# Kernel optimization log

Measured on AMD Instinct MI355X. Metric: run time of the kernel, lower is better.

The kernel has to match this reference:

```python
import jax, jax.numpy as jnp
import numpy as np

NEG_INF = -1e30

def _rotate_half(x):
    x1, x2 = jnp.split(x, 2, axis=-1)
    return jnp.concatenate([-x2, x1], axis=-1)

def _apply_rope(x, sin, cos):
    # x: [b, t, h, d]; sin/cos: [t, d]
    s = sin[None, :, None, :]
    c = cos[None, :, None, :]
    return x * c + _rotate_half(x) * s

def setup_inputs() -> dict:
    key = jax.random.key(0)
    ks = jax.random.split(key, 5)
    B, T, D, H = 2, 2048, 2048, 16
    hd = D // H
    x = jax.random.normal(ks[0], (B, T, D), dtype=jnp.float32)
    sin = jax.random.normal(ks[1], (T, hd), dtype=jnp.float32)
    cos = jax.random.normal(ks[2], (T, hd), dtype=jnp.float32)
    W_qkv = jax.random.normal(ks[3], (D, D + 2 * hd), dtype=jnp.float32) * (1.0 / np.sqrt(D))
    W_o = jax.random.normal(ks[4], (D, D), dtype=jnp.float32) * (1.0 / np.sqrt(D))
    return {"x": x, "sin": sin, "cos": cos, "W_qkv": W_qkv, "W_o": W_o}

def reference(x, sin, cos, W_qkv, W_o):
    B, T, D = x.shape
    num_heads = 16
    head_dim = D // num_heads
    scale = head_dim ** (-0.5)

    qkv = x @ W_qkv                              # [B, T, D + 2*hd]
    q, k, v = jnp.split(qkv, [D, D + head_dim], axis=-1)
    # q -> [B, H, T, hd]; k, v single KV head -> [B, 1, T, hd]
    q = q.reshape(B, T, num_heads, head_dim).transpose(0, 2, 1, 3)
    k = k[:, :, None, :].transpose(0, 2, 1, 3)   # [B, 1, T, hd]
    v = v[:, :, None, :].transpose(0, 2, 1, 3)

    # module scales q by head_dim^-0.5 BEFORE rope/attention
    q = q * scale

    # apply_rope_safe: transpose to [B, T, H, hd], apply rope, transpose back
    q = _apply_rope(q.transpose(0, 2, 1, 3), sin, cos).transpose(0, 2, 1, 3)
    k = _apply_rope(k.transpose(0, 2, 1, 3), sin, cos).transpose(0, 2, 1, 3)

    k0 = k[:, 0]                                 # [B, T, hd] (MQA shared KV)
    v0 = v[:, 0]

    # jax.nn.dot_product_attention applies its own 1/sqrt(hd) scaling on top
    scores = jnp.einsum('bhqd,bkd->bhqk', q, k0) * scale
    causal = jnp.tril(jnp.ones((T, T), dtype=bool))
    scores = jnp.where(causal[None, None], scores, NEG_INF)
    probs = jax.nn.softmax(scores, axis=-1)
    out = jnp.einsum('bhqk,bkd->bhqd', probs, v0)  # [B, H, T, hd]

    out = out.transpose(0, 2, 1, 3).reshape(B, T, D)
    return out @ W_o
```

## Files before the change

kernel.cpp:

```cpp
#include <hip/hip_runtime.h>
#include <stdint.h>

typedef __bf16 bf16x8_t __attribute__((ext_vector_type(8)));
typedef float f32x4_t __attribute__((ext_vector_type(4)));

#define AS1 __attribute__((address_space(1)))
#define AS3 __attribute__((address_space(3)))

static __device__ __forceinline__ unsigned short f2bf(float f) {
  union { float f; unsigned u; } a;
  a.f = f;
  unsigned r = a.u + 0x7fffu + ((a.u >> 16) & 1u);
  return (unsigned short)(r >> 16);
}

static __device__ __forceinline__ unsigned pack2bf(float lo, float hi) {
  return (unsigned)f2bf(lo) | ((unsigned)f2bf(hi) << 16);
}

__global__ void cvt_bf16_kernel(const float* __restrict__ in, unsigned short* __restrict__ out) {
  long i = ((long)blockIdx.x * blockDim.x + threadIdx.x) * 4;
  float4 v = *(const float4*)(in + i);
  ushort4 o;
  o.x = f2bf(v.x);
  o.y = f2bf(v.y);
  o.z = f2bf(v.z);
  o.w = f2bf(v.w);
  *(ushort4*)(out + i) = o;
}

__global__ void transpose_f32_bf16(const float* __restrict__ src, unsigned short* __restrict__ dst,
                                   int ld, int dld, long sbs, long dbs) {
  __shared__ float tile[64][65];
  src += (long)blockIdx.z * sbs;
  dst += (long)blockIdx.z * dbs;
  const int c0 = blockIdx.x * 64, r0 = blockIdx.y * 64;
  const int tx = threadIdx.x, ty = threadIdx.y;
#pragma unroll
  for (int j = 0; j < 64; j += 4)
    tile[ty + j][tx] = src[(long)(r0 + ty + j) * ld + (c0 + tx)];
  __syncthreads();
#pragma unroll
  for (int j = 0; j < 64; j += 4)
    dst[(long)(c0 + ty + j) * dld + (r0 + tx)] = f2bf(tile[tx][ty + j]);
}

__global__ __launch_bounds__(256) void gemm_bt(const unsigned short* __restrict__ A,
                                               const unsigned short* __restrict__ Bt,
                                               float* __restrict__ C,
                                               int M, int N, int K, int nx) {
  __shared__ unsigned short As[3][128 * 32];
  __shared__ unsigned short Bs[3][128 * 32];
  const int nwg = gridDim.x;
  const int bid = blockIdx.x;
  const int swz = (bid & 7) * (nwg >> 3) + (bid >> 3);
  const int by = swz / nx;
  const int bx = swz - by * nx;

  const int tid = threadIdx.x;
  const int wid = tid >> 6, lane = tid & 63;
  const int r16 = lane & 15, g = lane >> 4;
  const long bm = (long)by * 128;
  const long bn = (long)bx * 128;
  const int wr = (wid >> 1) * 64, wc = (wid & 1) * 64;
  const int gr = g ^ (r16 & 3);
  const int sslot = (lane & 3) ^ ((lane >> 2) & 3);

  f32x4_t acc[4][4];
#pragma unroll
  for (int i = 0; i < 4; i++)
#pragma unroll
    for (int j = 0; j < 4; j++) acc[i][j] = (f32x4_t){0.f, 0.f, 0.f, 0.f};

  const int NT = K >> 5;

#define STAGE_G(buf, kt)                                                              \
  {                                                                                   \
    _Pragma("unroll") for (int i = 0; i < 2; i++) {                                   \
      const int chunk = (i * 4 + wid) * 64 + lane;                                    \
      const int row = chunk >> 2;                                                     \
      __builtin_amdgcn_global_load_lds(                                               \
          (const AS1 void*)(A + (bm + row) * K + (kt) + sslot * 8),                   \
          (AS3 void*)(&As[buf][chunk * 8]), 16, 0, 0);                                \
      __builtin_amdgcn_global_load_lds(                                               \
          (const AS1 void*)(Bt + (bn + row) * K + (kt) + sslot * 8),                  \
          (AS3 void*)(&Bs[buf][chunk * 8]), 16, 0, 0);                                \
    }                                                                                 \
  }

  STAGE_G(0, 0)
  STAGE_G(1, 32)
  asm volatile("s_waitcnt vmcnt(4)" ::: "memory");
  __builtin_amdgcn_s_barrier();

  for (int T = 0; T < NT; T++) {
    const int cur = T % 3;
    if (T + 2 < NT) {
      const int nb = (T + 2) % 3;
      STAGE_G(nb, (T + 2) * 32)
    }
    __builtin_amdgcn_sched_barrier(0);
    bf16x8_t af[4], bfr[4];
#pragma unroll
    for (int mi = 0; mi < 4; mi++)
      af[mi] = *(const bf16x8_t*)(&As[cur][(wr + mi * 16 + r16) * 32 + gr * 8]);
#pragma unroll
    for (int ni = 0; ni < 4; ni++)
      bfr[ni] = *(const bf16x8_t*)(&Bs[cur][(wc + ni * 16 + r16) * 32 + gr * 8]);
    __builtin_amdgcn_s_setprio(1);
#pragma unroll
    for (int mi = 0; mi < 4; mi++)
#pragma unroll
      for (int ni = 0; ni < 4; ni++)
        acc[mi][ni] = __builtin_amdgcn_mfma_f32_16x16x32_bf16(af[mi], bfr[ni], acc[mi][ni], 0, 0, 0);
    __builtin_amdgcn_s_setprio(0);
    if (T + 2 < NT)
      asm volatile("s_waitcnt vmcnt(4)" ::: "memory");
    else
      asm volatile("s_waitcnt vmcnt(0)" ::: "memory");
    __builtin_amdgcn_s_barrier();
  }
#undef STAGE_G

#pragma unroll
  for (int mi = 0; mi < 4; mi++)
#pragma unroll
    for (int ni = 0; ni < 4; ni++) {
      const long rowb = bm + wr + mi * 16 + 4 * g;
      const long colb = bn + wc + ni * 16 + r16;
#pragma unroll
      for (int j = 0; j < 4; j++)
        C[(rowb + j) * N + colb] = acc[mi][ni][j];
    }
}

__global__ void rope_kernel(const float* __restrict__ qkv,
                            const float* __restrict__ sinp,
                            const float* __restrict__ cosp,
                            unsigned short* __restrict__ qr,
                            unsigned short* __restrict__ kr) {
  const int row = blockIdx.x;
  const int b = row >> 11, t = row & 2047;
  const float* src = qkv + (long)row * 2304;
  const int tid = threadIdx.x;
  const int d = tid & 127;
  const int dp = (d + 64) & 127;
  const float c = cosp[t * 128 + d];
  const float s = sinp[t * 128 + d];
  const float sgn = (d < 64) ? -1.f : 1.f;
  for (int h = (tid >> 7); h < 16; h += 2) {
    const float x0 = src[h * 128 + d];
    const float xp = src[h * 128 + dp];
    qr[((long)((b * 16 + h) * 2048 + t)) * 128 + d] = f2bf((x0 * c + sgn * xp * s) * 0.0078125f);
  }
  if (tid < 128) {
    const float x0 = src[2048 + d];
    const float xp = src[2048 + dp];
    kr[((long)(b * 2048 + t)) * 128 + d] = f2bf(x0 * c + sgn * xp * s);
  }
}

__global__ __launch_bounds__(256, 2)
void mqa_attn(const unsigned short* __restrict__ qr,
              const unsigned short* __restrict__ kr,
              const unsigned short* __restrict__ vT,
              unsigned short* __restrict__ ao) {
  __shared__ unsigned short Kb[2][64 * 128];
  __shared__ unsigned short Vb[128 * 64];
  __shared__ unsigned short plds[4][32 * 64];
  const int idx = blockIdx.x;
  const int bh = idx & 31, h = bh & 15, b = bh >> 4;
  const int chunk = idx >> 5;
  const int tile = 2 * (chunk & 7) + (chunk >> 3);
  const int tid = threadIdx.x;
  const int wid = tid >> 6, lane = tid & 63;
  const int r = lane & 15, g = lane >> 4;
  const int rs = r & 7;
  char* pw = (char*)&plds[wid][0];

  const unsigned short* kbase = kr + (long)b * 2048 * 128;
  const unsigned short* vbase = vT + (long)b * 128 * 2048;
  const unsigned short* qh = qr + (long)(b * 16 + h) * 2048 * 128;

  const int scol = (tid & 15) ^ ((tid >> 4) & 7);
  const int vscol = (tid & 7) ^ ((tid >> 3) & 7);

  f32x4_t o[2][8];
#pragma unroll
  for (int qg = 0; qg < 2; qg++)
#pragma unroll
    for (int i = 0; i < 8; i++) o[qg][i] = (f32x4_t){0.f, 0.f, 0.f, 0.f};
  float m0 = 0.f, m1 = 0.f, ls0 = 0.f, ls1 = 0.f;

  bf16x8_t qf[2][4];
#pragma unroll
  for (int qg = 0; qg < 2; qg++) {
    const unsigned short* qp = qh + (long)(tile * 128 + wid * 32 + qg * 16 + r) * 128 + g * 8;
#pragma unroll
    for (int c = 0; c < 4; c++) qf[qg][c] = *(const bf16x8_t*)(qp + c * 32);
  }

#pragma unroll
  for (int i = 0; i < 4; i++) {
    const int row = i * 16 + (tid >> 4);
    __builtin_amdgcn_global_load_lds(
        (const AS1 void*)(kbase + (long)row * 128 + scol * 8),
        (AS3 void*)(&Kb[0][(i * 256 + tid) * 8]), 16, 0, 0);
  }
  asm volatile("s_waitcnt vmcnt(0)" ::: "memory");
  __builtin_amdgcn_s_barrier();

  const int nstg = 2 * tile + 2;
  for (int s = 0; s < nstg; s++) {
    const int cur = s & 1;
    const int kv0 = 64 * s;

#pragma unroll
    for (int i = 0; i < 4; i++) {
      const int vrow = i * 32 + (tid >> 3);
      __builtin_amdgcn_global_load_lds(
          (const AS1 void*)(vbase + (long)vrow * 2048 + kv0 + vscol * 8),
          (AS3 void*)(&Vb[(i * 256 + tid) * 8]), 16, 0, 0);
    }
    if (s + 1 < nstg) {
      const int kvn = 64 * (s + 1);
#pragma unroll
      for (int i = 0; i < 4; i++) {
        const int row = i * 16 + (tid >> 4);
        __builtin_amdgcn_global_load_lds(
            (const AS1 void*)(kbase + (long)(kvn + row) * 128 + scol * 8),
            (AS3 void*)(&Kb[cur ^ 1][(i * 256 + tid) * 8]), 16, 0, 0);
      }
    }
    __builtin_amdgcn_sched_barrier(0);

    f32x4_t sc[2][4];
#pragma unroll
    for (int qg = 0; qg < 2; qg++)
#pragma unroll
      for (int t = 0; t < 4; t++) sc[qg][t] = (f32x4_t){0.f, 0.f, 0.f, 0.f};
    const unsigned short* Kcur = &Kb[cur][0];
    __builtin_amdgcn_s_setprio(1);
#pragma unroll
    for (int t = 0; t < 4; t++) {
      const unsigned short* krow = Kcur + (16 * t + r) * 128;
#pragma unroll
      for (int c = 0; c < 4; c++) {
        const bf16x8_t kf = *(const bf16x8_t*)(krow + (((4 * c + g) ^ rs) << 3));
        sc[0][t] = __builtin_amdgcn_mfma_f32_16x16x32_bf16(kf, qf[0][c], sc[0][t], 0, 0, 0);
        sc[1][t] = __builtin_amdgcn_mfma_f32_16x16x32_bf16(kf, qf[1][c], sc[1][t], 0, 0, 0);
      }
    }
    __builtin_amdgcn_s_setprio(0);

    if (s >= 2 * tile) {
      const int sub = s - 2 * tile;
#pragma unroll
      for (int qg = 0; qg < 2; qg++)
#pragma unroll
        for (int t = 0; t < 4; t++)
#pragma unroll
          for (int jj = 0; jj < 4; jj++)
            if (64 * sub + 16 * t + 4 * g + jj > wid * 32 + qg * 16 + r) sc[qg][t][jj] = -1e30f;
    }
    float lm0 = sc[0][0][0], lm1 = sc[1][0][0];
#pragma unroll
    for (int t = 0; t < 4; t++)
#pragma unroll
      for (int jj = 0; jj < 4; jj++) {
        lm0 = fmaxf(lm0, sc[0][t][jj]);
        lm1 = fmaxf(lm1, sc[1][t][jj]);
      }
    if (!__all(lm0 <= m0 + 8.f && lm1 <= m1 + 8.f)) {
      float pm0 = lm0, pm1 = lm1;
      pm0 = fmaxf(pm0, __shfl_xor(pm0, 16));
      pm0 = fmaxf(pm0, __shfl_xor(pm0, 32));
      pm1 = fmaxf(pm1, __shfl_xor(pm1, 16));
      pm1 = fmaxf(pm1, __shfl_xor(pm1, 32));
      const float mn0 = fmaxf(m0, pm0), mn1 = fmaxf(m1, pm1);
      const float a0 = __expf(m0 - mn0), a1 = __expf(m1 - mn1);
      ls0 *= a0;
      ls1 *= a1;
      float aj0[4], aj1[4];
#pragma unroll
      for (int jj = 0; jj < 4; jj++) {
        aj0[jj] = __shfl(a0, 4 * g + jj);
        aj1[jj] = __shfl(a1, 4 * g + jj);
      }
#pragma unroll
      for (int dt = 0; dt < 8; dt++)
#pragma unroll
        for (int jj = 0; jj < 4; jj++) {
          o[0][dt][jj] *= aj0[jj];
          o[1][dt][jj] *= aj1[jj];
        }
      m0 = mn0;
      m1 = mn1;
    }
    float p0[16], p1[16];
#pragma unroll
    for (int t = 0; t < 4; t++)
#pragma unroll
      for (int jj = 0; jj < 4; jj++) {
        p0[4 * t + jj] = __expf(sc[0][t][jj] - m0);
        p1[4 * t + jj] = __expf(sc[1][t][jj] - m1);
      }
    float a0 = 0.f, a1 = 0.f;
#pragma unroll
    for (int i = 0; i < 16; i++) {
      a0 += p0[i];
      a1 += p1[i];
    }
    ls0 += a0;
    ls1 += a1;

    asm volatile("" ::: "memory");
#pragma unroll
    for (int t = 0; t < 4; t++) {
      uint2 w0 = {pack2bf(p0[4 * t], p0[4 * t + 1]), pack2bf(p0[4 * t + 2], p0[4 * t + 3])};
      uint2 w1 = {pack2bf(p1[4 * t], p1[4 * t + 1]), pack2bf(p1[4 * t + 2], p1[4 * t + 3])};
      const int slot = (((2 * t + (g >> 1)) ^ rs) << 4) + ((g & 1) << 3);
      *(uint2*)(pw + r * 128 + slot) = w0;
      *(uint2*)(pw + (16 + r) * 128 + slot) = w1;
    }
    asm volatile("s_waitcnt lgkmcnt(0)" ::: "memory");
    const bf16x8_t pa00 = *(const bf16x8_t*)(pw + r * 128 + ((g ^ rs) << 4));
    const bf16x8_t pa01 = *(const bf16x8_t*)(pw + r * 128 + (((4 + g) ^ rs) << 4));
    const bf16x8_t pa10 = *(const bf16x8_t*)(pw + (16 + r) * 128 + ((g ^ rs) << 4));
    const bf16x8_t pa11 = *(const bf16x8_t*)(pw + (16 + r) * 128 + (((4 + g) ^ rs) << 4));

    if (s + 1 < nstg)
      asm volatile("s_waitcnt vmcnt(4)" ::: "memory");
    else
      asm volatile("s_waitcnt vmcnt(0)" ::: "memory");
    __builtin_amdgcn_s_barrier();

    __builtin_amdgcn_s_setprio(1);
#pragma unroll
    for (int dt = 0; dt < 8; dt++) {
      const bf16x8_t vfA = *(const bf16x8_t*)(Vb + (dt * 16 + r) * 64 + ((g ^ rs) << 3));
      o[0][dt] = __builtin_amdgcn_mfma_f32_16x16x32_bf16(pa00, vfA, o[0][dt], 0, 0, 0);
      o[1][dt] = __builtin_amdgcn_mfma_f32_16x16x32_bf16(pa10, vfA, o[1][dt], 0, 0, 0);
    }
#pragma unroll
    for (int dt = 0; dt < 8; dt++) {
      const bf16x8_t vfB = *(const bf16x8_t*)(Vb + (dt * 16 + r) * 64 + (((4 + g) ^ rs) << 3));
      o[0][dt] = __builtin_amdgcn_mfma_f32_16x16x32_bf16(pa01, vfB, o[0][dt], 0, 0, 0);
      o[1][dt] = __builtin_amdgcn_mfma_f32_16x16x32_bf16(pa11, vfB, o[1][dt], 0, 0, 0);
    }
    __builtin_amdgcn_s_setprio(0);

    asm volatile("s_waitcnt vmcnt(0)" ::: "memory");
    __builtin_amdgcn_s_barrier();
  }
#pragma unroll
  for (int qg = 0; qg < 2; qg++) {
    float lt = (qg == 0) ? ls0 : ls1;
    lt += __shfl_xor(lt, 16);
    lt += __shfl_xor(lt, 32);
    float rl[4];
#pragma unroll
    for (int jj = 0; jj < 4; jj++) rl[jj] = 1.0f / __shfl(lt, 4 * g + jj);
    unsigned short* aop =
        ao + ((long)(b * 2048 + tile * 128 + wid * 32 + qg * 16 + 4 * g)) * 2048 + h * 128 + r;
#pragma unroll
    for (int dt = 0; dt < 8; dt++)
#pragma unroll
      for (int jj = 0; jj < 4; jj++)
        aop[(long)jj * 2048 + dt * 16] = f2bf(o[qg][dt][jj] * rl[jj]);
  }
}

extern "C" void kernel_launch(void* const* d_in, const int* in_sizes, int n_in,
                              void* d_out, int out_size, void* d_ws, size_t ws_size,
                              hipStream_t stream) {
  const float* x    = (const float*)d_in[0];
  const float* sinp = (const float*)d_in[1];
  const float* cosp = (const float*)d_in[2];
  const float* Wqkv = (const float*)d_in[3];
  const float* Wo   = (const float*)d_in[4];
  float* out = (float*)d_out;
  char* ws = (char*)d_ws;

  const int B = 2, T = 2048, D = 2048, H = 16, HD = 128;
  const int M = B * T;
  const int NQ = D + 2 * HD;

  unsigned short* xb    = (unsigned short*)(ws + 0);
  unsigned short* wqkvT = (unsigned short*)(ws + 16777216);
  unsigned short* woT   = (unsigned short*)(ws + 26214400);
  float*          qkv   = (float*)         (ws + 34603008);
  unsigned short* qr    = (unsigned short*)(ws + 72351744);
  unsigned short* kr    = (unsigned short*)(ws + 89128960);
  unsigned short* vT    = (unsigned short*)(ws + 90177536);
  unsigned short* ao    = xb;

  dim3 tb(64, 4);
  cvt_bf16_kernel<<<(M * D) / 1024, 256, 0, stream>>>(x, xb);
  transpose_f32_bf16<<<dim3(NQ / 64, D / 64, 1), tb, 0, stream>>>(Wqkv, wqkvT, NQ, D, 0, 0);
  transpose_f32_bf16<<<dim3(D / 64, D / 64, 1), tb, 0, stream>>>(Wo, woT, D, D, 0, 0);
  gemm_bt<<<dim3((NQ / 128) * (M / 128)), 256, 0, stream>>>(xb, wqkvT, qkv, M, NQ, D, NQ / 128);
  rope_kernel<<<M, 256, 0, stream>>>(qkv, sinp, cosp, qr, kr);
  transpose_f32_bf16<<<dim3(HD / 64, T / 64, B), tb, 0, stream>>>(
      qkv + 2176, vT, NQ, T, (long)T * NQ, (long)HD * T);
  mqa_attn<<<dim3(512), 256, 0, stream>>>(qr, kr, vT, ao);
  gemm_bt<<<dim3((D / 128) * (M / 128)), 256, 0, stream>>>(ao, woT, out, M, D, D, D / 128);
}
```

Baseline: 224.3 us.

## Pair causal query tiles per block to balance attention work

Each attention block now handles two query tiles, p and 15-p, so every block runs exactly 34 KV stages. This replaces the 512-block grid of uneven causal work with 256 equally loaded blocks, and the pipelined K/V prefetch carries across the tile switch. Launch bounds drop to one block per SIMD-occupancy target, which gives more registers but less latency hiding. With 256 blocks on a 256-CU part there is one block per CU and no tail imbalance, at the cost of lower occupancy.

```diff
diff --git a/kernel.cpp b/kernel.cpp
--- a/kernel.cpp
+++ b/kernel.cpp
@@ -160,7 +160,7 @@
   }
 }
 
-__global__ __launch_bounds__(256, 2)
+__global__ __launch_bounds__(256, 1)
 void mqa_attn(const unsigned short* __restrict__ qr,
               const unsigned short* __restrict__ kr,
               const unsigned short* __restrict__ vT,
@@ -170,8 +170,7 @@
   __shared__ unsigned short plds[4][32 * 64];
   const int idx = blockIdx.x;
   const int bh = idx & 31, h = bh & 15, b = bh >> 4;
-  const int chunk = idx >> 5;
-  const int tile = 2 * (chunk & 7) + (chunk >> 3);
+  const int p = idx >> 5;
   const int tid = threadIdx.x;
   const int wid = tid >> 6, lane = tid & 63;
   const int r = lane & 15, g = lane >> 4;
@@ -186,19 +185,48 @@
   const int vscol = (tid & 7) ^ ((tid >> 3) & 7);
 
   f32x4_t o[2][8];
-#pragma unroll
-  for (int qg = 0; qg < 2; qg++)
-#pragma unroll
-    for (int i = 0; i < 8; i++) o[qg][i] = (f32x4_t){0.f, 0.f, 0.f, 0.f};
-  float m0 = 0.f, m1 = 0.f, ls0 = 0.f, ls1 = 0.f;
-
+  float m0, m1, ls0, ls1;
   bf16x8_t qf[2][4];
-#pragma unroll
-  for (int qg = 0; qg < 2; qg++) {
-    const unsigned short* qp = qh + (long)(tile * 128 + wid * 32 + qg * 16 + r) * 128 + g * 8;
-#pragma unroll
-    for (int c = 0; c < 4; c++) qf[qg][c] = *(const bf16x8_t*)(qp + c * 32);
-  }
+  int tile = p;
+  const int switch_s = 2 * p + 2;
+
+  auto load_q = [&]() {
+#pragma unroll
+    for (int qg = 0; qg < 2; qg++) {
+      const unsigned short* qp = qh + (long)(tile * 128 + wid * 32 + qg * 16 + r) * 128 + g * 8;
+#pragma unroll
+      for (int c = 0; c < 4; c++) qf[qg][c] = *(const bf16x8_t*)(qp + c * 32);
+    }
+  };
+  auto reset_state = [&]() {
+#pragma unroll
+    for (int qg = 0; qg < 2; qg++)
+#pragma unroll
+      for (int i = 0; i < 8; i++) o[qg][i] = (f32x4_t){0.f, 0.f, 0.f, 0.f};
+    m0 = m1 = 0.f;
+    ls0 = ls1 = 0.f;
+  };
+  auto flush = [&]() {
+#pragma unroll
+    for (int qg = 0; qg < 2; qg++) {
+      float lt = (qg == 0) ? ls0 : ls1;
+      lt += __shfl_xor(lt, 16);
+      lt += __shfl_xor(lt, 32);
+      float rl[4];
+#pragma unroll
+      for (int jj = 0; jj < 4; jj++) rl[jj] = 1.0f / __shfl(lt, 4 * g + jj);
+      unsigned short* aop =
+          ao + ((long)(b * 2048 + tile * 128 + wid * 32 + qg * 16 + 4 * g)) * 2048 + h * 128 + r;
+#pragma unroll
+      for (int dt = 0; dt < 8; dt++)
+#pragma unroll
+        for (int jj = 0; jj < 4; jj++)
+          aop[(long)jj * 2048 + dt * 16] = f2bf(o[qg][dt][jj] * rl[jj]);
+    }
+  };
+
+  load_q();
+  reset_state();
 
 #pragma unroll
   for (int i = 0; i < 4; i++) {
@@ -210,10 +238,16 @@
   asm volatile("s_waitcnt vmcnt(0)" ::: "memory");
   __builtin_amdgcn_s_barrier();
 
-  const int nstg = 2 * tile + 2;
-  for (int s = 0; s < nstg; s++) {
+  for (int s = 0; s < 34; s++) {
     const int cur = s & 1;
-    const int kv0 = 64 * s;
+    if (s == switch_s) {
+      flush();
+      tile = 15 - p;
+      load_q();
+      reset_state();
+    }
+    const int ss = (s < switch_s) ? s : s - switch_s;
+    const int kv0 = 64 * ss;
 
 #pragma unroll
     for (int i = 0; i < 4; i++) {
@@ -222,8 +256,9 @@
           (const AS1 void*)(vbase + (long)vrow * 2048 + kv0 + vscol * 8),
           (AS3 void*)(&Vb[(i * 256 + tid) * 8]), 16, 0, 0);
     }
-    if (s + 1 < nstg) {
-      const int kvn = 64 * (s + 1);
+    const int ns = s + 1;
+    if (ns < 34) {
+      const int kvn = (ns < switch_s) ? 64 * ns : 64 * (ns - switch_s);
 #pragma unroll
       for (int i = 0; i < 4; i++) {
         const int row = i * 16 + (tid >> 4);
@@ -253,8 +288,8 @@
     }
     __builtin_amdgcn_s_setprio(0);
 
-    if (s >= 2 * tile) {
-      const int sub = s - 2 * tile;
+    if (ss >= 2 * tile) {
+      const int sub = ss - 2 * tile;
 #pragma unroll
       for (int qg = 0; qg < 2; qg++)
 #pragma unroll
@@ -329,7 +364,7 @@
     const bf16x8_t pa10 = *(const bf16x8_t*)(pw + (16 + r) * 128 + ((g ^ rs) << 4));
     const bf16x8_t pa11 = *(const bf16x8_t*)(pw + (16 + r) * 128 + (((4 + g) ^ rs) << 4));
 
-    if (s + 1 < nstg)
+    if (ns < 34)
       asm volatile("s_waitcnt vmcnt(4)" ::: "memory");
     else
       asm volatile("s_waitcnt vmcnt(0)" ::: "memory");
@@ -353,22 +388,7 @@
     asm volatile("s_waitcnt vmcnt(0)" ::: "memory");
     __builtin_amdgcn_s_barrier();
   }
-#pragma unroll
-  for (int qg = 0; qg < 2; qg++) {
-    float lt = (qg == 0) ? ls0 : ls1;
-    lt += __shfl_xor(lt, 16);
-    lt += __shfl_xor(lt, 32);
-    float rl[4];
-#pragma unroll
-    for (int jj = 0; jj < 4; jj++) rl[jj] = 1.0f / __shfl(lt, 4 * g + jj);
-    unsigned short* aop =
-        ao + ((long)(b * 2048 + tile * 128 + wid * 32 + qg * 16 + 4 * g)) * 2048 + h * 128 + r;
-#pragma unroll
-    for (int dt = 0; dt < 8; dt++)
-#pragma unroll
-      for (int jj = 0; jj < 4; jj++)
-        aop[(long)jj * 2048 + dt * 16] = f2bf(o[qg][dt][jj] * rl[jj]);
-  }
+  flush();
 }
 
 extern "C" void kernel_launch(void* const* d_in, const int* in_sizes, int n_in,
@@ -403,6 +423,6 @@
   rope_kernel<<<M, 256, 0, stream>>>(qkv, sinp, cosp, qr, kr);
   transpose_f32_bf16<<<dim3(HD / 64, T / 64, B), tb, 0, stream>>>(
       qkv + 2176, vT, NQ, T, (long)T * NQ, (long)HD * T);
-  mqa_attn<<<dim3(512), 256, 0, stream>>>(qr, kr, vT, ao);
+  mqa_attn<<<dim3(256), 256, 0, stream>>>(qr, kr, vT, ao);
   gemm_bt<<<dim3((D / 128) * (M / 128)), 256, 0, stream>>>(ao, woT, out, M, D, D, D / 128);
 }
```

Result: no change. 225.0 us (+0.3%).
